# Kernel optimization log

Hardware: AMD Instinct MI355X
Metric: run time of the kernel (lower is better)

Reference implementation:

```python
import jax, jax.numpy as jnp
import numpy as np

TD_MAX = 1024  # matches init_kwargs td_max; ensemble_average=True


def setup_inputs() -> dict:
    key = jax.random.key(0)
    # trajectory: [T_frames, N_particles, 3]
    x = jax.random.normal(key, (4096, 2048, 3), dtype=jnp.float32)
    return {"x": x}


def reference(x):
    # Original (ensemble_average=True):
    #   MSD[td] = (1/n_t0) * sum_{t0=0}^{n_t0-1} mean_{n,d} (x[t0+td] - x[t0])^2
    # Since every t0 window has the same (N,3) size, this equals a single
    # mean over (t0, n, d) per lag td. We scan over lags to avoid
    # materializing the full [td_max, n_t0, N, 3] gather.
    T = x.shape[0]
    n_t0 = T - TD_MAX
    base = x[:n_t0]  # [n_t0, N, 3] shared origin frames

    def per_lag(carry, td):
        win = jax.lax.dynamic_slice_in_dim(x, td, n_t0, axis=0)  # [n_t0, N, 3]
        d = win - base
        return carry, jnp.mean(d * d)

    _, msd = jax.lax.scan(per_lag, None, jnp.arange(TD_MAX))
    return msd  # [td_max]
```

## Files before the change

kernel.cpp:

```cpp
#include <hip/hip_runtime.h>

#define T_TOTAL 4096
#define NT0     3072
#define CH      6144
#define TD_MAXL 1024

#define KS     4
#define KC     (CH / KS)
#define BK     32
#define NSTEP  (KC / BK)
#define NTI    24
#define ND     9
#define NTILE  (NTI * ND)
#define NBLK   (NTILE * KS)
#define LDH    40

typedef _Float16 half8 __attribute__((ext_vector_type(8)));
typedef float    f32x4 __attribute__((ext_vector_type(4)));


__global__ __launch_bounds__(256) void init_kernel(float* __restrict__ Cbuf) {
    int i = blockIdx.x * 256 + threadIdx.x;
    if (i < TD_MAXL) Cbuf[i] = 0.0f;
}

__global__ __launch_bounds__(256) void s_kernel(const float* __restrict__ x,
                                                float* __restrict__ S) {
    const int t = blockIdx.x;
    const float4* row = (const float4*)(x + (size_t)t * CH);
    float s = 0.f;
    for (int k = threadIdx.x; k < CH / 4; k += 256) {
        float4 v = row[k];
        s = fmaf(v.x, v.x, s);
        s = fmaf(v.y, v.y, s);
        s = fmaf(v.z, v.z, s);
        s = fmaf(v.w, v.w, s);
    }
    #pragma unroll
    for (int off = 32; off >= 1; off >>= 1) s += __shfl_xor(s, off, 64);
    __shared__ float part[4];
    const int lane = threadIdx.x & 63, wid = threadIdx.x >> 6;
    if (lane == 0) part[wid] = s;
    __syncthreads();
    if (threadIdx.x == 0) S[t] = part[0] + part[1] + part[2] + part[3];
}

__device__ inline half8 pack8(const float4 u, const float4 v) {
    half8 h;
    h[0] = (_Float16)u.x; h[1] = (_Float16)u.y; h[2] = (_Float16)u.z; h[3] = (_Float16)u.w;
    h[4] = (_Float16)v.x; h[5] = (_Float16)v.y; h[6] = (_Float16)v.z; h[7] = (_Float16)v.w;
    return h;
}

__global__ __launch_bounds__(256, 2) void cross_mfma(const float* __restrict__ x,
                                                     float* __restrict__ C) {
    __shared__ _Float16 As[2][128][LDH];
    __shared__ _Float16 Bs[2][128][LDH];
    __shared__ float    C_loc[256];

    const int tid = threadIdx.x;

    const int bid  = blockIdx.x;
    const int xcd  = bid & 7;
    const int slot = bid >> 3;
    const int ks   = slot / 27;
    const int tt   = slot % 27;
    const int tile = xcd * 27 + tt;
    const int I    = tile / ND;
    const int D    = tile % ND;
    const int i0 = I * 128, j0 = (I + D) * 128;
    const int k0 = ks * KC;

    C_loc[tid] = 0.f;

    const int srow = tid >> 1;
    const int skq  = (tid & 1) << 4;
    const float* gA = x + (size_t)(i0 + srow) * CH + k0 + skq;
    const float* gB = x + (size_t)(j0 + srow) * CH + k0 + skq;

    const int lane = tid & 63, wid = tid >> 6;
    const int wm = wid >> 1, wn = wid & 1;
    const int fr = lane & 15, ss = lane >> 4;
    const int rowA = wm * 64 + fr;
    const int rowB = wn * 64 + fr;

    f32x4 acc[4][4];
    #pragma unroll
    for (int m = 0; m < 4; ++m)
        #pragma unroll
        for (int n = 0; n < 4; ++n) acc[m][n] = (f32x4)0.f;

    {
        float4 a[4], b[4];
        #pragma unroll
        for (int q = 0; q < 4; ++q) {
            a[q] = ((const float4*)gA)[q];
            b[q] = ((const float4*)gB)[q];
        }
        *(half8*)&As[0][srow][skq]     = pack8(a[0], a[1]);
        *(half8*)&As[0][srow][skq + 8] = pack8(a[2], a[3]);
        *(half8*)&Bs[0][srow][skq]     = pack8(b[0], b[1]);
        *(half8*)&Bs[0][srow][skq + 8] = pack8(b[2], b[3]);
    }

    int cur = 0;
    for (int t = 0; t < NSTEP; ++t) {
        float4 a[4], b[4];
        const bool more = (t + 1 < NSTEP);
        if (more) {
            const float* pA = gA + (size_t)(t + 1) * BK;
            const float* pB = gB + (size_t)(t + 1) * BK;
            #pragma unroll
            for (int q = 0; q < 4; ++q) {
                a[q] = ((const float4*)pA)[q];
                b[q] = ((const float4*)pB)[q];
            }
        }
        __syncthreads();

        half8 fA[4], fB[4];
        #pragma unroll
        for (int m = 0; m < 4; ++m)
            fA[m] = *(const half8*)&As[cur][rowA + 16 * m][ss * 8];
        #pragma unroll
        for (int n = 0; n < 4; ++n)
            fB[n] = *(const half8*)&Bs[cur][rowB + 16 * n][ss * 8];
        #pragma unroll
        for (int m = 0; m < 4; ++m)
            #pragma unroll
            for (int n = 0; n < 4; ++n)
                acc[m][n] = __builtin_amdgcn_mfma_f32_16x16x32_f16(fA[m], fB[n],
                                                                   acc[m][n], 0, 0, 0);
        if (more) {
            const int nb = cur ^ 1;
            *(half8*)&As[nb][srow][skq]     = pack8(a[0], a[1]);
            *(half8*)&As[nb][srow][skq + 8] = pack8(a[2], a[3]);
            *(half8*)&Bs[nb][srow][skq]     = pack8(b[0], b[1]);
            *(half8*)&Bs[nb][srow][skq + 8] = pack8(b[2], b[3]);
        }
        cur ^= 1;
    }

    float buck[7][4];
    #pragma unroll
    for (int dd = 0; dd < 7; ++dd)
        #pragma unroll
        for (int rr = 0; rr < 4; ++rr) buck[dd][rr] = 0.f;
    #pragma unroll
    for (int m = 0; m < 4; ++m)
        #pragma unroll
        for (int n = 0; n < 4; ++n)
            #pragma unroll
            for (int rr = 0; rr < 4; ++rr)
                buck[n - m + 3][rr] += acc[m][n][rr];

    const int obase = 64 * (wn - wm) + 128 + (fr - (ss << 2));
    #pragma unroll
    for (int dd = 0; dd < 7; ++dd)
        #pragma unroll
        for (int rr = 0; rr < 4; ++rr)
            atomicAdd(&C_loc[obase + 16 * (dd - 3) - rr], buck[dd][rr]);
    __syncthreads();

    const int td = D * 128 + tid - 128;
    if (td >= 0 && td < TD_MAXL) atomicAdd(&C[td], C_loc[tid]);
}

__global__ __launch_bounds__(256) void combine_kernel(const float* __restrict__ S,
                                                      const float* __restrict__ C,
                                                      float* __restrict__ out) {
    const int td = blockIdx.x;
    float p = 0.f, q = 0.f;
    for (int t = threadIdx.x; t < NT0; t += 256) {
        p += S[t + td];
        q += S[t];
    }
    #pragma unroll
    for (int off = 32; off >= 1; off >>= 1) {
        p += __shfl_xor(p, off, 64);
        q += __shfl_xor(q, off, 64);
    }
    __shared__ float pp[4], qq[4];
    const int lane = threadIdx.x & 63, wid = threadIdx.x >> 6;
    if (lane == 0) { pp[wid] = p; qq[wid] = q; }
    __syncthreads();
    if (threadIdx.x == 0) {
        const float P = pp[0] + pp[1] + pp[2] + pp[3];
        const float Q = qq[0] + qq[1] + qq[2] + qq[3];
        const float inv_M = 1.0f / ((float)NT0 * (float)CH);
        out[td] = (P + Q - 2.0f * C[td]) * inv_M;
    }
}

extern "C" void kernel_launch(void* const* d_in, const int* in_sizes, int n_in,
                              void* d_out, int out_size, void* d_ws, size_t ws_size,
                              hipStream_t stream) {
    const float* x = (const float*)d_in[0];
    float* out = (float*)d_out;
    float* S = (float*)d_ws;
    float* C = S + T_TOTAL;

    init_kernel<<<dim3((TD_MAXL + 255) / 256), dim3(256), 0, stream>>>(C);
    s_kernel<<<dim3(T_TOTAL), dim3(256), 0, stream>>>(x, S);
    cross_mfma<<<dim3(NBLK), dim3(256), 0, stream>>>(x, C);
    combine_kernel<<<dim3(TD_MAXL), dim3(256), 0, stream>>>(S, C, out);
}
```

Before: 281.6 us.

## Use 32x32 MFMA, split K eightfold, prefix-sum S, fold init kernel

The cross kernel now uses 32x32x16 f16 MFMA tiles instead of 16x16x32 and splits K into 8 chunks instead of 4, which doubles the block count for better occupancy across CUs. The diagonal accumulation reuses the A-tile LDS buffer instead of a separate array. The per-lag combine kernel, which re-summed S for every lag, is replaced by a single-block double-precision prefix scan plus a tiny final kernel. C zeroing is folded into s_kernel, which removes one launch. Trade-offs: more global atomics on C and a serial scan kernel on one block.

```diff
diff --git a/kernel.cpp b/kernel.cpp
--- a/kernel.cpp
+++ b/kernel.cpp
@@ -5,7 +5,7 @@
 #define CH      6144
 #define TD_MAXL 1024
 
-#define KS     4
+#define KS     8
 #define KC     (CH / KS)
 #define BK     32
 #define NSTEP  (KC / BK)
@@ -15,18 +15,15 @@
 #define NBLK   (NTILE * KS)
 #define LDH    40
 
-typedef _Float16 half8 __attribute__((ext_vector_type(8)));
-typedef float    f32x4 __attribute__((ext_vector_type(4)));
-
-
-__global__ __launch_bounds__(256) void init_kernel(float* __restrict__ Cbuf) {
-    int i = blockIdx.x * 256 + threadIdx.x;
-    if (i < TD_MAXL) Cbuf[i] = 0.0f;
-}
+typedef _Float16 half8  __attribute__((ext_vector_type(8)));
+typedef float    f32x16 __attribute__((ext_vector_type(16)));
+
 
 __global__ __launch_bounds__(256) void s_kernel(const float* __restrict__ x,
-                                                float* __restrict__ S) {
+                                                float* __restrict__ S,
+                                                float* __restrict__ C) {
     const int t = blockIdx.x;
+    if (t < TD_MAXL && threadIdx.x == 0) C[t] = 0.0f;
     const float4* row = (const float4*)(x + (size_t)t * CH);
     float s = 0.f;
     for (int k = threadIdx.x; k < CH / 4; k += 256) {
@@ -45,6 +42,31 @@
     if (threadIdx.x == 0) S[t] = part[0] + part[1] + part[2] + part[3];
 }
 
+__global__ __launch_bounds__(256) void scan_kernel(const float* __restrict__ S,
+                                                   double* __restrict__ PS) {
+    __shared__ double sh[256];
+    const int tid = threadIdx.x;
+    double run = 0.0;
+    #pragma unroll
+    for (int j = 0; j < 16; ++j) run += (double)S[16 * tid + j];
+    sh[tid] = run;
+    __syncthreads();
+    for (int off = 1; off < 256; off <<= 1) {
+        double tv = (tid >= off) ? sh[tid - off] : 0.0;
+        __syncthreads();
+        sh[tid] += tv;
+        __syncthreads();
+    }
+    double base = (tid == 0) ? 0.0 : sh[tid - 1];
+    if (tid == 0) PS[0] = 0.0;
+    double r = base;
+    #pragma unroll
+    for (int j = 0; j < 16; ++j) {
+        r += (double)S[16 * tid + j];
+        PS[16 * tid + j + 1] = r;
+    }
+}
+
 __device__ inline half8 pack8(const float4 u, const float4 v) {
     half8 h;
     h[0] = (_Float16)u.x; h[1] = (_Float16)u.y; h[2] = (_Float16)u.z; h[3] = (_Float16)u.w;
@@ -56,11 +78,9 @@
                                                      float* __restrict__ C) {
     __shared__ _Float16 As[2][128][LDH];
     __shared__ _Float16 Bs[2][128][LDH];
-    __shared__ float    C_loc[256];
 
     const int tid = threadIdx.x;
-
-    const int bid  = blockIdx.x;
+    const int bid = blockIdx.x;
     const int xcd  = bid & 7;
     const int slot = bid >> 3;
     const int ks   = slot / 27;
@@ -71,8 +91,6 @@
     const int i0 = I * 128, j0 = (I + D) * 128;
     const int k0 = ks * KC;
 
-    C_loc[tid] = 0.f;
-
     const int srow = tid >> 1;
     const int skq  = (tid & 1) << 4;
     const float* gA = x + (size_t)(i0 + srow) * CH + k0 + skq;
@@ -80,15 +98,13 @@
 
     const int lane = tid & 63, wid = tid >> 6;
     const int wm = wid >> 1, wn = wid & 1;
-    const int fr = lane & 15, ss = lane >> 4;
-    const int rowA = wm * 64 + fr;
-    const int rowB = wn * 64 + fr;
-
-    f32x4 acc[4][4];
-    #pragma unroll
-    for (int m = 0; m < 4; ++m)
-        #pragma unroll
-        for (int n = 0; n < 4; ++n) acc[m][n] = (f32x4)0.f;
+    const int r32 = lane & 31, hi = lane >> 5;
+
+    f32x16 acc[2][2];
+    #pragma unroll
+    for (int m = 0; m < 2; ++m)
+        #pragma unroll
+        for (int n = 0; n < 2; ++n) acc[m][n] = (f32x16)0.f;
 
     {
         float4 a[4], b[4];
@@ -118,19 +134,27 @@
         }
         __syncthreads();
 
-        half8 fA[4], fB[4];
-        #pragma unroll
-        for (int m = 0; m < 4; ++m)
-            fA[m] = *(const half8*)&As[cur][rowA + 16 * m][ss * 8];
-        #pragma unroll
-        for (int n = 0; n < 4; ++n)
-            fB[n] = *(const half8*)&Bs[cur][rowB + 16 * n][ss * 8];
-        #pragma unroll
-        for (int m = 0; m < 4; ++m)
-            #pragma unroll
-            for (int n = 0; n < 4; ++n)
-                acc[m][n] = __builtin_amdgcn_mfma_f32_16x16x32_f16(fA[m], fB[n],
+        half8 fA[2][2], fB[2][2];
+        #pragma unroll
+        for (int m = 0; m < 2; ++m)
+            #pragma unroll
+            for (int kk = 0; kk < 2; ++kk)
+                fA[m][kk] = *(const half8*)&As[cur][wm * 64 + m * 32 + r32][kk * 16 + hi * 8];
+        #pragma unroll
+        for (int n = 0; n < 2; ++n)
+            #pragma unroll
+            for (int kk = 0; kk < 2; ++kk)
+                fB[n][kk] = *(const half8*)&Bs[cur][wn * 64 + n * 32 + r32][kk * 16 + hi * 8];
+        #pragma unroll
+        for (int m = 0; m < 2; ++m)
+            #pragma unroll
+            for (int n = 0; n < 2; ++n) {
+                acc[m][n] = __builtin_amdgcn_mfma_f32_32x32x16_f16(fA[m][0], fB[n][0],
                                                                    acc[m][n], 0, 0, 0);
+                acc[m][n] = __builtin_amdgcn_mfma_f32_32x32x16_f16(fA[m][1], fB[n][1],
+                                                                   acc[m][n], 0, 0, 0);
+            }
+
         if (more) {
             const int nb = cur ^ 1;
             *(half8*)&As[nb][srow][skq]     = pack8(a[0], a[1]);
@@ -141,55 +165,35 @@
         cur ^= 1;
     }
 
-    float buck[7][4];
-    #pragma unroll
-    for (int dd = 0; dd < 7; ++dd)
-        #pragma unroll
-        for (int rr = 0; rr < 4; ++rr) buck[dd][rr] = 0.f;
-    #pragma unroll
-    for (int m = 0; m < 4; ++m)
-        #pragma unroll
-        for (int n = 0; n < 4; ++n)
-            #pragma unroll
-            for (int rr = 0; rr < 4; ++rr)
-                buck[n - m + 3][rr] += acc[m][n][rr];
-
-    const int obase = 64 * (wn - wm) + 128 + (fr - (ss << 2));
-    #pragma unroll
-    for (int dd = 0; dd < 7; ++dd)
-        #pragma unroll
-        for (int rr = 0; rr < 4; ++rr)
-            atomicAdd(&C_loc[obase + 16 * (dd - 3) - rr], buck[dd][rr]);
+    __syncthreads();
+    float* C_loc = (float*)&As[0][0][0];
+    C_loc[tid] = 0.f;
+    __syncthreads();
+
+    const int base = 128 + 64 * (wn - wm) + (r32 - 4 * hi);
+    f32x16 accD = acc[0][0] + acc[1][1];
+    #pragma unroll
+    for (int reg = 0; reg < 16; ++reg) {
+        const int rr = (reg & 3) + 8 * (reg >> 2);
+        atomicAdd(&C_loc[base - rr],      accD[reg]);
+        atomicAdd(&C_loc[base + 32 - rr], acc[0][1][reg]);
+        atomicAdd(&C_loc[base - 32 - rr], acc[1][0][reg]);
+    }
     __syncthreads();
 
     const int td = D * 128 + tid - 128;
     if (td >= 0 && td < TD_MAXL) atomicAdd(&C[td], C_loc[tid]);
 }
 
-__global__ __launch_bounds__(256) void combine_kernel(const float* __restrict__ S,
-                                                      const float* __restrict__ C,
-                                                      float* __restrict__ out) {
-    const int td = blockIdx.x;
-    float p = 0.f, q = 0.f;
-    for (int t = threadIdx.x; t < NT0; t += 256) {
-        p += S[t + td];
-        q += S[t];
-    }
-    #pragma unroll
-    for (int off = 32; off >= 1; off >>= 1) {
-        p += __shfl_xor(p, off, 64);
-        q += __shfl_xor(q, off, 64);
-    }
-    __shared__ float pp[4], qq[4];
-    const int lane = threadIdx.x & 63, wid = threadIdx.x >> 6;
-    if (lane == 0) { pp[wid] = p; qq[wid] = q; }
-    __syncthreads();
-    if (threadIdx.x == 0) {
-        const float P = pp[0] + pp[1] + pp[2] + pp[3];
-        const float Q = qq[0] + qq[1] + qq[2] + qq[3];
-        const float inv_M = 1.0f / ((float)NT0 * (float)CH);
-        out[td] = (P + Q - 2.0f * C[td]) * inv_M;
-    }
+__global__ __launch_bounds__(256) void final_kernel(const double* __restrict__ PS,
+                                                    const float* __restrict__ C,
+                                                    float* __restrict__ out) {
+    const int td = blockIdx.x * 256 + threadIdx.x;
+    if (td >= TD_MAXL) return;
+    const double P = PS[td + NT0] - PS[td];
+    const double Q = PS[NT0];
+    const double inv_M = 1.0 / ((double)NT0 * (double)CH);
+    out[td] = (float)((P + Q - 2.0 * (double)C[td]) * inv_M);
 }
 
 extern "C" void kernel_launch(void* const* d_in, const int* in_sizes, int n_in,
@@ -197,11 +201,12 @@
                               hipStream_t stream) {
     const float* x = (const float*)d_in[0];
     float* out = (float*)d_out;
-    float* S = (float*)d_ws;
-    float* C = S + T_TOTAL;
-
-    init_kernel<<<dim3((TD_MAXL + 255) / 256), dim3(256), 0, stream>>>(C);
-    s_kernel<<<dim3(T_TOTAL), dim3(256), 0, stream>>>(x, S);
+    float*  S  = (float*)d_ws;
+    float*  C  = S + T_TOTAL;
+    double* PS = (double*)((char*)d_ws + 20480);
+
+    s_kernel<<<dim3(T_TOTAL), dim3(256), 0, stream>>>(x, S, C);
+    scan_kernel<<<dim3(1), dim3(256), 0, stream>>>(S, PS);
     cross_mfma<<<dim3(NBLK), dim3(256), 0, stream>>>(x, C);
-    combine_kernel<<<dim3(TD_MAXL), dim3(256), 0, stream>>>(S, C, out);
-}
+    final_kernel<<<dim3(TD_MAXL / 256), dim3(256), 0, stream>>>(PS, C, out);
+}
```

After: 335.4 us. +19.1%, slower.
